# Performance work log

Hardware: AMD Instinct MI355X
Metric: run time of the kernel (lower is better)

The kernel has to match this reference:

```python
import jax, jax.numpy as jnp
import numpy as np

B, T, D, H, E = 4, 2048, 768, 3072, 8


def setup_inputs() -> dict:
    key = jax.random.key(0)
    ks = jax.random.split(key, 7)
    s_d = 1.0 / np.sqrt(D)
    s_h = 1.0 / np.sqrt(H)
    return {
        "x": jax.random.normal(ks[0], (B, T, D), dtype=jnp.float32),
        # gate: Linear(D, E). (Original inits to zero; random here for nontrivial routing.)
        "Wg": jax.random.normal(ks[1], (E, D), dtype=jnp.float32) * s_d,
        "bg": jax.random.normal(ks[2], (E,), dtype=jnp.float32) * 0.01,
        # stacked expert MLPs: Linear(D,H) -> GELU(exact) -> Linear(H,D)
        "W1": jax.random.normal(ks[3], (E, D, H), dtype=jnp.float32) * s_d,
        "b1": jax.random.normal(ks[4], (E, H), dtype=jnp.float32) * s_d,
        "W2": jax.random.normal(ks[5], (E, H, D), dtype=jnp.float32) * s_h,
        "b2": jax.random.normal(ks[6], (E, D), dtype=jnp.float32) * s_h,
    }


def reference(x, Wg, bg, W1, b1, W2, b2):
    b, t, d = x.shape
    xf = x.reshape(-1, d)                      # [N, D]
    n = xf.shape[0]
    logits = xf @ Wg.T + bg                    # [N, E]
    probs = jax.nn.softmax(logits, axis=-1)
    top2_vals, top2_idx = jax.lax.top_k(probs, 2)  # [N, 2]
    # combine weights: cw[n, e] = top2 prob if expert e is in token n's top-2 else 0
    cw = jnp.zeros((n, Wg.shape[0]), dtype=x.dtype)
    cw = cw.at[jnp.arange(n)[:, None], top2_idx].set(top2_vals)
    # per-expert MLP on all tokens (zero combine weight kills non-routed experts)
    h = jax.nn.gelu(jnp.einsum('nd,edh->neh', xf, W1) + b1[None], approximate=False)
    y = jnp.einsum('neh,ehd->ned', h, W2) + b2[None]   # [N, E, D]
    out = jnp.einsum('ne,ned->nd', cw, y)
    return out.reshape(b, t, d)
```

## Files before the change

### kernel.cpp

```cpp
#include <hip/hip_runtime.h>
#include <hip/hip_bf16.h>
#include <math.h>

#define E_EXPERTS 8
#define D_DIM 768
#define H_DIM 3072
#define N_TOK 8192
#define SLOTS (2 * N_TOK)
#define SCAT_BLOCKS 32
#define MB_L 20

typedef unsigned short ushort_t;
typedef __attribute__((ext_vector_type(8))) __bf16 bf16x8;
typedef __attribute__((ext_vector_type(4))) float f32x4;

__device__ __forceinline__ unsigned short f2bf(float f) {
    unsigned int u = __float_as_uint(f);
    unsigned int r = (u + 0x7FFFu + ((u >> 16) & 1u)) >> 16;
    return (unsigned short)r;
}

__device__ __forceinline__ void gload_lds16(const void* g, void* l) {
    __builtin_amdgcn_global_load_lds(
        (const __attribute__((address_space(1))) unsigned int*)g,
        (__attribute__((address_space(3))) unsigned int*)l, 16, 0, 0);
}


__global__ void transpose_conv_kernel(const float* __restrict__ src, ushort_t* __restrict__ dst,
                                      int R, int C) {
    __shared__ float tile[64][65];
    int e = blockIdx.z;
    const float* S = src + (size_t)e * R * C;
    ushort_t* Dp = dst + (size_t)e * R * C;
    int c0 = blockIdx.x * 64, r0 = blockIdx.y * 64;
    int tx = threadIdx.x & 15, ty = threadIdx.x >> 4;
#pragma unroll
    for (int p = 0; p < 4; p++) {
        float4 v = *(const float4*)&S[(size_t)(r0 + ty + 16 * p) * C + c0 + tx * 4];
        tile[ty + 16 * p][tx * 4 + 0] = v.x;
        tile[ty + 16 * p][tx * 4 + 1] = v.y;
        tile[ty + 16 * p][tx * 4 + 2] = v.z;
        tile[ty + 16 * p][tx * 4 + 3] = v.w;
    }
    __syncthreads();
#pragma unroll
    for (int p = 0; p < 4; p++) {
        int cc = ty + 16 * p;
        int rr = tx * 4;
        ushort4 o;
        o.x = f2bf(tile[rr + 0][cc]);
        o.y = f2bf(tile[rr + 1][cc]);
        o.z = f2bf(tile[rr + 2][cc]);
        o.w = f2bf(tile[rr + 3][cc]);
        *(ushort4*)&Dp[(size_t)(c0 + cc) * R + r0 + rr] = o;
    }
}


__global__ void gate_kernel(const float* __restrict__ x, const float* __restrict__ Wg,
                            const float* __restrict__ bg, ushort_t* __restrict__ xb,
                            int* __restrict__ top_idx, float* __restrict__ top_w) {
    int w = threadIdx.x >> 6, lane = threadIdx.x & 63;
    int t = blockIdx.x * 4 + w;
    if (t >= N_TOK) return;
    const float* xr = x + (size_t)t * D_DIM;
    float xs[12];
#pragma unroll
    for (int j = 0; j < 12; j++) xs[j] = xr[lane + 64 * j];
#pragma unroll
    for (int j = 0; j < 12; j++) xb[(size_t)t * D_DIM + lane + 64 * j] = f2bf(xs[j]);
    float pr[8];
#pragma unroll
    for (int ee = 0; ee < 8; ee++) {
        const float* wr = Wg + ee * D_DIM;
        float p = 0.f;
#pragma unroll
        for (int j = 0; j < 12; j++) p += xs[j] * wr[lane + 64 * j];
#pragma unroll
        for (int o = 32; o > 0; o >>= 1) p += __shfl_xor(p, o);
        pr[ee] = p + bg[ee];
    }
    float mx = pr[0];
#pragma unroll
    for (int ee = 1; ee < 8; ee++) mx = fmaxf(mx, pr[ee]);
    float s = 0.f;
#pragma unroll
    for (int ee = 0; ee < 8; ee++) { pr[ee] = expf(pr[ee] - mx); s += pr[ee]; }
    float inv = 1.f / s;
#pragma unroll
    for (int ee = 0; ee < 8; ee++) pr[ee] *= inv;
    int i0 = 0;
#pragma unroll
    for (int ee = 1; ee < 8; ee++) if (pr[ee] > pr[i0]) i0 = ee;
    int i1 = -1;
#pragma unroll
    for (int ee = 0; ee < 8; ee++) {
        if (ee == i0) continue;
        if (i1 < 0 || pr[ee] > pr[i1]) i1 = ee;
    }
    if (lane == 0) {
        top_idx[2 * t] = i0;
        top_idx[2 * t + 1] = i1;
        top_w[2 * t] = pr[i0];
        top_w[2 * t + 1] = pr[i1];
    }
}

__global__ void hist_kernel(const int* __restrict__ top_idx, int* __restrict__ bc) {
    __shared__ int h[E_EXPERTS];
    if (threadIdx.x < E_EXPERTS) h[threadIdx.x] = 0;
    __syncthreads();
    int t = blockIdx.x * 256 + threadIdx.x;
    atomicAdd(&h[top_idx[2 * t]], 1);
    atomicAdd(&h[top_idx[2 * t + 1]], 1);
    __syncthreads();
    if (threadIdx.x < E_EXPERTS) bc[blockIdx.x * E_EXPERTS + threadIdx.x] = h[threadIdx.x];
}

__global__ void scan_kernel(const int* __restrict__ bc, int* __restrict__ counts,
                            int* __restrict__ offsets, int* __restrict__ base) {
    int tid = threadIdx.x;
    if (tid < E_EXPERTS) {
        int acc = 0;
        for (int b = 0; b < SCAT_BLOCKS; b++) {
            base[b * E_EXPERTS + tid] = acc;
            acc += bc[b * E_EXPERTS + tid];
        }
        counts[tid] = acc;
    }
    __syncthreads();
    if (tid == 0) {
        int acc = 0;
        for (int e = 0; e < E_EXPERTS; e++) { offsets[e] = acc; acc += counts[e]; }
    }
    __syncthreads();
    if (tid < E_EXPERTS) {
        int o = offsets[tid];
        for (int b = 0; b < SCAT_BLOCKS; b++) base[b * E_EXPERTS + tid] += o;
    }
}

__global__ void scatter_kernel(const int* __restrict__ top_idx, const float* __restrict__ top_w,
                               const int* __restrict__ base, int* __restrict__ perm,
                               float* __restrict__ wgt, int* __restrict__ tok2slot) {
    __shared__ int cur[E_EXPERTS];
    if (threadIdx.x < E_EXPERTS) cur[threadIdx.x] = 0;
    __syncthreads();
    int t = blockIdx.x * 256 + threadIdx.x;
#pragma unroll
    for (int sl = 0; sl < 2; sl++) {
        int ee = top_idx[2 * t + sl];
        int p = atomicAdd(&cur[ee], 1);
        int s = base[blockIdx.x * E_EXPERTS + ee] + p;
        perm[s] = t;
        wgt[s] = top_w[2 * t + sl];
        tok2slot[2 * t + sl] = s;
    }
}

__global__ void combine_kernel(const float* __restrict__ y, const int* __restrict__ tok2slot,
                               float* __restrict__ out) {
    int idx = blockIdx.x * blockDim.x + threadIdx.x;
    int stride = gridDim.x * blockDim.x;
    const int QR = D_DIM / 4;
    for (int i = idx; i < N_TOK * QR; i += stride) {
        int t = i / QR, d4 = i - t * QR;
        int s0 = tok2slot[2 * t], s1 = tok2slot[2 * t + 1];
        float4 a = ((const float4*)(y + (size_t)s0 * D_DIM))[d4];
        float4 b = ((const float4*)(y + (size_t)s1 * D_DIM))[d4];
        float4 o;
        o.x = a.x + b.x; o.y = a.y + b.y; o.z = a.z + b.z; o.w = a.w + b.w;
        ((float4*)(out + (size_t)t * D_DIM))[d4] = o;
    }
}

template <int MODE>
__global__ __launch_bounds__(256, 2) void moe_gemm_kernel(
    const ushort_t* __restrict__ A, const ushort_t* __restrict__ BT,
    const float* __restrict__ bias, const int* __restrict__ offsets,
    const int* __restrict__ counts, const int* __restrict__ perm,
    const float* __restrict__ wgt, ushort_t* __restrict__ Hout, float* __restrict__ Y) {
    constexpr int K = (MODE == 0) ? D_DIM : H_DIM;
    constexpr int N = (MODE == 0) ? H_DIM : D_DIM;
    constexpr int KT = K / 64;
    constexpr int NB = N / 128;

    const int wgid = blockIdx.x;
    const int c = wgid & 7;
    const int r = wgid >> 3;
    const int mb = r % MB_L;
    const int q = r / MB_L;
    const int g = q * 8 + c;
    const int e = g / NB;
    const int nb = g % NB;

    const int ne = counts[e];
    const int m0 = mb * 128;
    if (m0 >= ne) return;
    const int n0 = nb * 128;
    const int base = offsets[e];
    const ushort_t* Bt = BT + (size_t)e * ((size_t)N * K);

    __shared__ alignas(16) ushort_t As[2 * 128 * 64];
    __shared__ alignas(16) ushort_t Bs[2 * 128 * 64];

    const int tid = threadIdx.x;
    const int lane = tid & 63;
    const int w = tid >> 6;
    const int wm = w >> 1, wn = w & 1;
    const int lr = lane & 15, lk = (lane >> 4) * 8;
    const int gx = lr & 7;

    const int r0s = tid >> 3;
    const int c8 = (((tid & 7) ^ ((tid >> 3) & 7)) * 8);
    int aoff[2][2], boff[2][2];
#pragma unroll
    for (int H = 0; H < 2; H++)
#pragma unroll
        for (int i = 0; i < 2; i++) {
            int trow = H * 64 + r0s + i * 32;
            int rcl = min(m0 + trow, ne - 1);
            int arow = (MODE == 0) ? perm[base + rcl] : (base + rcl);
            aoff[H][i] = arow * K + c8;
            boff[H][i] = (n0 + trow) * K + c8;
        }

    auto stageA = [&](int tt, int H) {
#pragma unroll
        for (int i = 0; i < 2; i++)
            gload_lds16(A + (size_t)aoff[H][i] + (size_t)tt * 64,
                        &As[(tt & 1) * 8192 + H * 4096 + (w * 64 + i * 256) * 8]);
    };
    auto stageB = [&](int tt, int H) {
#pragma unroll
        for (int i = 0; i < 2; i++)
            gload_lds16(Bt + (size_t)boff[H][i] + (size_t)tt * 64,
                        &Bs[(tt & 1) * 8192 + H * 4096 + (w * 64 + i * 256) * 8]);
    };

    f32x4 acc[4][4];
#pragma unroll
    for (int i = 0; i < 4; i++)
#pragma unroll
        for (int j = 0; j < 4; j++) acc[i][j] = (f32x4){0.f, 0.f, 0.f, 0.f};

    stageA(0, 0); stageA(0, 1);
    stageB(0, 0); stageB(0, 1);
    stageB(1, 0); stageB(1, 1);
    asm volatile("s_waitcnt vmcnt(4)" ::: "memory");
    __builtin_amdgcn_s_barrier();

    const int colK0 = (((0 * 4) + (lk >> 3)) ^ gx) << 3;
    const int colK1 = (((1 * 4) + (lk >> 3)) ^ gx) << 3;

    bf16x8 bfr[4][2];
    for (int t = 0; t < KT; ++t) {
        const int sl = (t & 1) * 8192;
#pragma unroll
        for (int p = 0; p < 2; ++p) {
            bf16x8 af[2][2];
            if (p == 0) {
#pragma unroll
                for (int fc = 0; fc < 4; fc++) {
                    int R = wn * 64 + fc * 16 + lr;
                    int roff = sl + (R >> 6) * 4096 + (R & 63) * 64;
                    bfr[fc][0] = *(const bf16x8*)&Bs[roff + colK0];
                    bfr[fc][1] = *(const bf16x8*)&Bs[roff + colK1];
                }
            }
#pragma unroll
            for (int pl = 0; pl < 2; pl++) {
                int R = wm * 64 + (2 * p + pl) * 16 + lr;
                int roff = sl + (R >> 6) * 4096 + (R & 63) * 64;
                af[pl][0] = *(const bf16x8*)&As[roff + colK0];
                af[pl][1] = *(const bf16x8*)&As[roff + colK1];
            }
            if (p == 0 && t + 1 < KT) { stageA(t + 1, 0); stageA(t + 1, 1); }
            if (p == 1 && t + 2 < KT) { stageB(t + 2, 0); stageB(t + 2, 1); }
            __builtin_amdgcn_s_barrier();
            asm volatile("s_waitcnt lgkmcnt(0)" ::: "memory");
            __builtin_amdgcn_s_setprio(1);
#pragma unroll
            for (int pl = 0; pl < 2; pl++)
#pragma unroll
                for (int fc = 0; fc < 4; fc++)
#pragma unroll
                    for (int kk = 0; kk < 2; kk++)
                        acc[2 * p + pl][fc] = __builtin_amdgcn_mfma_f32_16x16x32_bf16(
                            af[pl][kk], bfr[fc][kk], acc[2 * p + pl][fc], 0, 0, 0);
            __builtin_amdgcn_s_setprio(0);
            if (p == 1) {
                if (t + 2 < KT) asm volatile("s_waitcnt vmcnt(4)" ::: "memory");
                else            asm volatile("s_waitcnt vmcnt(0)" ::: "memory");
            }
            __builtin_amdgcn_s_barrier();
        }
    }

    const int rg0 = (lane >> 4) * 4;
#pragma unroll
    for (int fr = 0; fr < 4; fr++) {
#pragma unroll
        for (int fc = 0; fc < 4; fc++) {
            int cn = n0 + wn * 64 + fc * 16 + lr;
            float bi = bias[e * N + cn];
            f32x4 v = acc[fr][fc];
#pragma unroll
            for (int rg = 0; rg < 4; rg++) {
                int rm = m0 + wm * 64 + fr * 16 + rg0 + rg;
                if (rm < ne) {
                    if (MODE == 0) {
                        float xv = v[rg] + bi;
                        float u = xv * 1.5957691216f * __builtin_fmaf(0.044715f * xv, xv, 1.0f);
                        float gl = xv / (1.f + __expf(-u));
                        Hout[(size_t)(base + rm) * H_DIM + cn] = f2bf(gl);
                    } else {
                        int s = base + rm;
                        float wv = wgt[s];
                        Y[(size_t)s * D_DIM + cn] = wv * (v[rg] + bi);
                    }
                }
            }
        }
    }
}


extern "C" void kernel_launch(void* const* d_in, const int* in_sizes, int n_in,
                              void* d_out, int out_size, void* d_ws, size_t ws_size,
                              hipStream_t stream) {
    const float* x  = (const float*)d_in[0];
    const float* Wg = (const float*)d_in[1];
    const float* bg = (const float*)d_in[2];
    const float* W1 = (const float*)d_in[3];
    const float* b1 = (const float*)d_in[4];
    const float* W2 = (const float*)d_in[5];
    const float* b2 = (const float*)d_in[6];
    float* out = (float*)d_out;

    char* p = (char*)d_ws;
    ushort_t* xb  = (ushort_t*)p; p += (size_t)N_TOK * D_DIM * 2;
    ushort_t* W1T = (ushort_t*)p; p += (size_t)E_EXPERTS * H_DIM * D_DIM * 2;
    ushort_t* W2T = (ushort_t*)p; p += (size_t)E_EXPERTS * D_DIM * H_DIM * 2;
    ushort_t* Hb  = (ushort_t*)p; p += (size_t)SLOTS * H_DIM * 2;
    int*   top_idx = (int*)p;   p += (size_t)N_TOK * 2 * 4;
    float* top_w   = (float*)p; p += (size_t)N_TOK * 2 * 4;
    int*   perm    = (int*)p;   p += (size_t)SLOTS * 4;
    float* wgt     = (float*)p; p += (size_t)SLOTS * 4;
    int*   t2s     = (int*)p;   p += (size_t)SLOTS * 4;
    int*   bc      = (int*)p;   p += SCAT_BLOCKS * E_EXPERTS * 4;
    int*   basep   = (int*)p;   p += SCAT_BLOCKS * E_EXPERTS * 4;
    int*   counts  = (int*)p;   p += 64;
    int*   offsets = (int*)p;   p += 64;
    float* y = (float*)d_ws;

    gate_kernel<<<N_TOK / 4, 256, 0, stream>>>(x, Wg, bg, xb, top_idx, top_w);
    transpose_conv_kernel<<<dim3(H_DIM / 64, D_DIM / 64, E_EXPERTS), 256, 0, stream>>>(W1, W1T, D_DIM, H_DIM);
    transpose_conv_kernel<<<dim3(D_DIM / 64, H_DIM / 64, E_EXPERTS), 256, 0, stream>>>(W2, W2T, H_DIM, D_DIM);
    hist_kernel<<<SCAT_BLOCKS, 256, 0, stream>>>(top_idx, bc);
    scan_kernel<<<1, 64, 0, stream>>>(bc, counts, offsets, basep);
    scatter_kernel<<<SCAT_BLOCKS, 256, 0, stream>>>(top_idx, top_w, basep, perm, wgt, t2s);
    moe_gemm_kernel<0><<<8 * MB_L * (H_DIM / 128), 256, 0, stream>>>(
        xb, W1T, b1, offsets, counts, perm, wgt, Hb, nullptr);
    moe_gemm_kernel<1><<<8 * MB_L * (D_DIM / 128), 256, 0, stream>>>(
        Hb, W2T, b2, offsets, counts, perm, wgt, nullptr, y);
    combine_kernel<<<2048, 256, 0, stream>>>(y, t2s, out);
}
```

Before: 353.9 us.

## Switch MoE GEMM to K=32 tiles with triple-buffered LDS pipeline

Restructures the expert GEMM main loop to use K-step 32 instead of 64, with a 3-stage ring of LDS buffers. Each iteration issues loads for the tile two steps ahead and does one barrier per step. A new rotation swizzle replaces the XOR layout, and launch bounds go from 2 to 3 blocks per CU. The smaller LDS footprint is meant to allow higher occupancy and better overlap of loads with MFMA, at the cost of twice as many loop iterations and barriers per tile.

```diff
diff --git a/kernel.cpp b/kernel.cpp
--- a/kernel.cpp
+++ b/kernel.cpp
@@ -176,14 +176,14 @@
 }
 
 template <int MODE>
-__global__ __launch_bounds__(256, 2) void moe_gemm_kernel(
+__global__ __launch_bounds__(256, 3) void moe_gemm_kernel(
     const ushort_t* __restrict__ A, const ushort_t* __restrict__ BT,
     const float* __restrict__ bias, const int* __restrict__ offsets,
     const int* __restrict__ counts, const int* __restrict__ perm,
     const float* __restrict__ wgt, ushort_t* __restrict__ Hout, float* __restrict__ Y) {
     constexpr int K = (MODE == 0) ? D_DIM : H_DIM;
     constexpr int N = (MODE == 0) ? H_DIM : D_DIM;
-    constexpr int KT = K / 64;
+    constexpr int KT = K / 32;
     constexpr int NB = N / 128;
 
     const int wgid = blockIdx.x;
@@ -202,42 +202,37 @@
     const int base = offsets[e];
     const ushort_t* Bt = BT + (size_t)e * ((size_t)N * K);
 
-    __shared__ alignas(16) ushort_t As[2 * 128 * 64];
-    __shared__ alignas(16) ushort_t Bs[2 * 128 * 64];
+    __shared__ alignas(16) ushort_t As[3 * 128 * 32];
+    __shared__ alignas(16) ushort_t Bs[3 * 128 * 32];
 
     const int tid = threadIdx.x;
     const int lane = tid & 63;
     const int w = tid >> 6;
     const int wm = w >> 1, wn = w & 1;
-    const int lr = lane & 15, lk = (lane >> 4) * 8;
-    const int gx = lr & 7;
-
-    const int r0s = tid >> 3;
-    const int c8 = (((tid & 7) ^ ((tid >> 3) & 7)) * 8);
-    int aoff[2][2], boff[2][2];
-#pragma unroll
-    for (int H = 0; H < 2; H++)
+    const int lr = lane & 15;
+    const int gq = lane >> 4;
+
+    int lds_dst[2];
+    int a_src[2], b_src[2];
+#pragma unroll
+    for (int i = 0; i < 2; i++) {
+        int s = 2 * w + i;
+        int row = s * 16 + (lane >> 2);
+        int lg = ((lane & 3) - (row >> 1)) & 3;
+        int rcl = min(m0 + row, ne - 1);
+        int arow = (MODE == 0) ? perm[base + rcl] : (base + rcl);
+        a_src[i] = arow * K + lg * 8;
+        b_src[i] = (n0 + row) * K + lg * 8;
+        lds_dst[i] = s * 512;
+    }
+
+    auto stage = [&](int tt, int bi) {
 #pragma unroll
         for (int i = 0; i < 2; i++) {
-            int trow = H * 64 + r0s + i * 32;
-            int rcl = min(m0 + trow, ne - 1);
-            int arow = (MODE == 0) ? perm[base + rcl] : (base + rcl);
-            aoff[H][i] = arow * K + c8;
-            boff[H][i] = (n0 + trow) * K + c8;
+            gload_lds16(A + (size_t)a_src[i] + (size_t)tt * 32, &As[bi * 4096 + lds_dst[i]]);
+            gload_lds16(Bt + (size_t)b_src[i] + (size_t)tt * 32, &Bs[bi * 4096 + lds_dst[i]]);
         }
-
-    auto stageA = [&](int tt, int H) {
-#pragma unroll
-        for (int i = 0; i < 2; i++)
-            gload_lds16(A + (size_t)aoff[H][i] + (size_t)tt * 64,
-                        &As[(tt & 1) * 8192 + H * 4096 + (w * 64 + i * 256) * 8]);
     };
-    auto stageB = [&](int tt, int H) {
-#pragma unroll
-        for (int i = 0; i < 2; i++)
-            gload_lds16(Bt + (size_t)boff[H][i] + (size_t)tt * 64,
-                        &Bs[(tt & 1) * 8192 + H * 4096 + (w * 64 + i * 256) * 8]);
-    };
 
     f32x4 acc[4][4];
 #pragma unroll
@@ -245,60 +240,39 @@
 #pragma unroll
         for (int j = 0; j < 4; j++) acc[i][j] = (f32x4){0.f, 0.f, 0.f, 0.f};
 
-    stageA(0, 0); stageA(0, 1);
-    stageB(0, 0); stageB(0, 1);
-    stageB(1, 0); stageB(1, 1);
+    stage(0, 0);
+    stage(1, 1);
     asm volatile("s_waitcnt vmcnt(4)" ::: "memory");
     __builtin_amdgcn_s_barrier();
 
-    const int colK0 = (((0 * 4) + (lk >> 3)) ^ gx) << 3;
-    const int colK1 = (((1 * 4) + (lk >> 3)) ^ gx) << 3;
-
-    bf16x8 bfr[4][2];
+    int cur = 0;
     for (int t = 0; t < KT; ++t) {
-        const int sl = (t & 1) * 8192;
-#pragma unroll
-        for (int p = 0; p < 2; ++p) {
-            bf16x8 af[2][2];
-            if (p == 0) {
-#pragma unroll
-                for (int fc = 0; fc < 4; fc++) {
-                    int R = wn * 64 + fc * 16 + lr;
-                    int roff = sl + (R >> 6) * 4096 + (R & 63) * 64;
-                    bfr[fc][0] = *(const bf16x8*)&Bs[roff + colK0];
-                    bfr[fc][1] = *(const bf16x8*)&Bs[roff + colK1];
-                }
-            }
-#pragma unroll
-            for (int pl = 0; pl < 2; pl++) {
-                int R = wm * 64 + (2 * p + pl) * 16 + lr;
-                int roff = sl + (R >> 6) * 4096 + (R & 63) * 64;
-                af[pl][0] = *(const bf16x8*)&As[roff + colK0];
-                af[pl][1] = *(const bf16x8*)&As[roff + colK1];
-            }
-            if (p == 0 && t + 1 < KT) { stageA(t + 1, 0); stageA(t + 1, 1); }
-            if (p == 1 && t + 2 < KT) { stageB(t + 2, 0); stageB(t + 2, 1); }
-            __builtin_amdgcn_s_barrier();
-            asm volatile("s_waitcnt lgkmcnt(0)" ::: "memory");
-            __builtin_amdgcn_s_setprio(1);
-#pragma unroll
-            for (int pl = 0; pl < 2; pl++)
-#pragma unroll
-                for (int fc = 0; fc < 4; fc++)
-#pragma unroll
-                    for (int kk = 0; kk < 2; kk++)
-                        acc[2 * p + pl][fc] = __builtin_amdgcn_mfma_f32_16x16x32_bf16(
-                            af[pl][kk], bfr[fc][kk], acc[2 * p + pl][fc], 0, 0, 0);
-            __builtin_amdgcn_s_setprio(0);
-            if (p == 1) {
-                if (t + 2 < KT) asm volatile("s_waitcnt vmcnt(4)" ::: "memory");
-                else            asm volatile("s_waitcnt vmcnt(0)" ::: "memory");
-            }
-            __builtin_amdgcn_s_barrier();
+        int sb = cur + 2; if (sb >= 3) sb -= 3;
+        if (t + 2 < KT) stage(t + 2, sb);
+        bf16x8 af[4], bfr[4];
+#pragma unroll
+        for (int f = 0; f < 4; f++) {
+            int Ra = wm * 64 + f * 16 + lr;
+            int Rb = wn * 64 + f * 16 + lr;
+            af[f]  = *(const bf16x8*)&As[cur * 4096 + Ra * 32 + (((gq + (Ra >> 1)) & 3) << 3)];
+            bfr[f] = *(const bf16x8*)&Bs[cur * 4096 + Rb * 32 + (((gq + (Rb >> 1)) & 3) << 3)];
         }
-    }
-
-    const int rg0 = (lane >> 4) * 4;
+        asm volatile("s_waitcnt lgkmcnt(0)" ::: "memory");
+        __builtin_amdgcn_s_setprio(1);
+#pragma unroll
+        for (int fm = 0; fm < 4; fm++)
+#pragma unroll
+            for (int fc = 0; fc < 4; fc++)
+                acc[fm][fc] = __builtin_amdgcn_mfma_f32_16x16x32_bf16(
+                    af[fm], bfr[fc], acc[fm][fc], 0, 0, 0);
+        __builtin_amdgcn_s_setprio(0);
+        if (t + 2 < KT) asm volatile("s_waitcnt vmcnt(4)" ::: "memory");
+        else            asm volatile("s_waitcnt vmcnt(0)" ::: "memory");
+        __builtin_amdgcn_s_barrier();
+        cur = (cur == 2) ? 0 : cur + 1;
+    }
+
+    const int rg0 = gq * 4;
 #pragma unroll
     for (int fr = 0; fr < 4; fr++) {
 #pragma unroll
```

Measured after the change: 395.4 us. 1.12x slower.
